# Optimization experiments

Hardware: AMD Instinct MI355X
Metric: run time of the kernel (lower is better)

The kernel has to match this reference:

```python
import jax, jax.numpy as jnp
import numpy as np

N = 4096          # residues
D = 256           # local feature dim
FACTOR = 2
H = 8             # global heads
DF = D * FACTOR   # 512
DH = DF // H      # 64 per-head dim
NUM_CHAINS = 64
NUM_BATCHES = 8


def index_mean(x, idx, mask, num_segments):
    """Masked segment mean, gathered back to per-element shape.
    x: [N, ...], idx: [N] int, mask: broadcastable to x (0/1)."""
    m = mask.astype(x.dtype)
    xm = x * m
    s = jax.ops.segment_sum(xm, idx, num_segments=num_segments)
    c = jax.ops.segment_sum(jnp.broadcast_to(m, x.shape), idx, num_segments=num_segments)
    mean = s / jnp.maximum(c, 1e-6)
    return mean[idx]


def setup_inputs() -> dict:
    key = jax.random.key(0)
    ks = jax.random.split(key, 12)
    s_in = 1.0 / np.sqrt(D)
    s_mid = 1.0 / np.sqrt(2 * DF)
    return {
        "local": jax.random.normal(ks[0], (N, D), jnp.float32),
        "chain": jax.random.randint(ks[1], (N,), 0, NUM_CHAINS),
        "batch": jax.random.randint(ks[2], (N,), 0, NUM_BATCHES),
        "mask": jax.random.bernoulli(ks[3], 0.9, (N,)),
        "W_key": jax.random.normal(ks[4], (D, DF), jnp.float32) * s_in,
        "b_key": jnp.zeros((DF,), jnp.float32),
        "W_value": jax.random.normal(ks[5], (D, DF), jnp.float32) * s_in,
        "b_value": jnp.zeros((DF,), jnp.float32),
        "W_query": jax.random.normal(ks[6], (D, DF), jnp.float32) * s_in,
        "b_query": jnp.zeros((DF,), jnp.float32),
        "W_bias": jax.random.normal(ks[7], (D, 2 * DF), jnp.float32) * s_in,
        "b_bias": jnp.zeros((2 * DF,), jnp.float32),
        "W_out": jax.random.normal(ks[8], (2 * DF, D), jnp.float32) * s_mid,
    }


def reference(local, chain, batch, mask,
              W_key, b_key, W_value, b_value, W_query, b_query,
              W_bias, b_bias, W_out):
    n = local.shape[0]
    k = jax.nn.gelu(local @ W_key + b_key).reshape(n, H, DH)
    v = (local @ W_value + b_value).reshape(n, H, DH)
    q = jax.nn.gelu(local @ W_query + b_query).reshape(n, H, DH)

    bias = index_mean(local @ W_bias + b_bias, batch, mask[:, None], NUM_BATCHES)

    # outer product key (x) value: [N, H, DH, DH]
    ov = k[:, :, :, None] * v[:, :, None, :]
    m4 = mask[:, None, None, None]
    chain_op = index_mean(ov, chain, m4, NUM_CHAINS)
    batch_op = index_mean(ov, batch, m4, NUM_BATCHES)
    operation = jnp.concatenate((chain_op, batch_op), axis=-2)  # [N, H, 2*DH, DH]

    out = jnp.einsum('bhvk,bhk->bhv', operation, q).reshape(n, -1) + bias
    return out @ W_out
```

## Files before the change

### kernel.cpp

```cpp
#include <hip/hip_runtime.h>
#include <math.h>

#define NN 4096
#define DD 256
#define DFF 512
#define HH 8
#define DHH 64
#define CAP_C 256
#define CAP_B 1024

#define OFF_KB     0
#define OFF_VB     1048576
#define OFF_QB     2097152
#define OFF_ATTNB  3145728
#define OFF_LOCALB 5242880
#define OFF_STC    5767168
#define OFF_STBP   7864320
#define OFF_BSUM   8912896
#define OFF_CNT    8921088
#define OFF_WQKVT  8921344
#define OFF_WOUTT  9117952
#define OFF_LISTS  9249024
#define OFF_LPART  9298176

typedef __attribute__((ext_vector_type(8))) short bf16x8;
typedef __attribute__((ext_vector_type(4))) float floatx4;

__device__ __forceinline__ float gelu_f(float x) {
    const float c = 0.7978845608028654f;
    float t = tanhf(c * (x + 0.044715f * x * x * x));
    return 0.5f * x * (1.0f + t);
}

__device__ __forceinline__ unsigned short f2b(float f) {
    union { float f; unsigned int u; } v; v.f = f;
    unsigned int r = (v.u + 0x7FFFu + ((v.u >> 16) & 1u)) >> 16;
    return (unsigned short)r;
}

__global__ __launch_bounds__(256) void prep_kernel(
    const float* __restrict__ local,
    const float* __restrict__ Wk, const float* __restrict__ Wv,
    const float* __restrict__ Wq, const float* __restrict__ Wout,
    const int* __restrict__ batch, const int* __restrict__ mask,
    unsigned short* __restrict__ Wqkvt, unsigned short* __restrict__ Woutt,
    unsigned short* __restrict__ localb,
    float* __restrict__ Lpart, float* __restrict__ zero_base)
{
    const int bid = blockIdx.x, tid = threadIdx.x;
    if (bid < 640) {
        const float* src; unsigned short* dst; int R, C, r0, c0;
        if (bid < 384) {
            int m = bid >> 7, ti = bid & 127;
            src = (m == 0) ? Wk : (m == 1) ? Wv : Wq;
            dst = Wqkvt + (size_t)m * 512 * 256;
            R = 256; C = 512;
            r0 = (ti >> 4) * 32; c0 = (ti & 15) * 32;
        } else {
            int ti = bid - 384;
            src = Wout; dst = Woutt;
            R = 1024; C = 256;
            r0 = (ti >> 3) * 32; c0 = (ti & 7) * 32;
        }
        __shared__ float Tl[32][33];
        int ty = tid >> 3, tx = tid & 7;
        float4 v = *(const float4*)(src + (size_t)(r0 + ty) * C + c0 + tx * 4);
        Tl[tx * 4 + 0][ty] = v.x;
        Tl[tx * 4 + 1][ty] = v.y;
        Tl[tx * 4 + 2][ty] = v.z;
        Tl[tx * 4 + 3][ty] = v.w;
        __syncthreads();
        ushort4 o;
        o.x = f2b(Tl[ty][tx * 4 + 0]);
        o.y = f2b(Tl[ty][tx * 4 + 1]);
        o.z = f2b(Tl[ty][tx * 4 + 2]);
        o.w = f2b(Tl[ty][tx * 4 + 3]);
        *(ushort4*)(dst + (size_t)(c0 + ty) * R + r0 + tx * 4) = o;
    } else if (bid < 704) {
        int p = bid - 640;
        float accl[8] = {};
        int n0 = p * 64;
        for (int r = 0; r < 64; ++r) {
            int n = n0 + r;
            float v = local[(size_t)n * DD + tid];
            int bb = batch[n];
            float vm = mask[n] ? v : 0.0f;
#pragma unroll
            for (int b = 0; b < 8; ++b)
                accl[b] += (bb == b) ? vm : 0.0f;
        }
#pragma unroll
        for (int b = 0; b < 8; ++b)
            Lpart[(size_t)p * 2048 + b * 256 + tid] = accl[b];
    } else if (bid < 1216) {
        int p = bid - 704;
        size_t base = (size_t)p * 2048 + tid * 8;
        float4 a0 = *(const float4*)(local + base);
        float4 a1 = *(const float4*)(local + base + 4);
        ushort4 p0, p1;
        p0.x = f2b(a0.x); p0.y = f2b(a0.y); p0.z = f2b(a0.z); p0.w = f2b(a0.w);
        p1.x = f2b(a1.x); p1.y = f2b(a1.y); p1.z = f2b(a1.z); p1.w = f2b(a1.w);
        *(ushort4*)(localb + base) = p0;
        *(ushort4*)(localb + base + 4) = p1;
    } else {
        float4 z4 = make_float4(0.f, 0.f, 0.f, 0.f);
        for (int i = tid; i < 2112; i += 256)
            ((float4*)zero_base)[i] = z4;
    }
}

__global__ __launch_bounds__(256) void qkv_kernel(
    const unsigned short* __restrict__ localb,
    const unsigned short* __restrict__ Wqkvt,
    const float* __restrict__ bk, const float* __restrict__ bv,
    const float* __restrict__ bq, unsigned short* __restrict__ KVQb,
    const int* __restrict__ chain, const int* __restrict__ batch,
    const int* __restrict__ mask, int* __restrict__ cnt,
    int* __restrict__ lists, const float* __restrict__ Lpart,
    const float* __restrict__ Wbias, float* __restrict__ Bsum)
{
    __shared__ __align__(16) char smem[36864];
    const int u = blockIdx.x, tid = threadIdx.x;
    int* cntc_m   = cnt;
    int* cntc_all = cnt + 64;
    int* cntb_m   = cnt + 128;
    int* cntb_all = cnt + 136;
    int* listc_m   = lists;
    int* listc_all = listc_m + 64 * CAP_C;
    int* listb_m   = listc_all + 64 * CAP_C;
    int* listb_all = listb_m + 8 * CAP_B;

    if (u < 384) {
        typedef unsigned short (*t72)[72];
        t72 Asl = (t72)smem;
        t72 Bsl = (t72)(smem + 18432);
        const int wave = tid >> 6, lane = tid & 63;
        const int kq = lane >> 4, la = lane & 15;
        const int cx = u % 12, ry = u / 12;
        const int row0 = ry * 128, cg0 = cx * 128;
        const int wrow = (wave & 1) * 64, wcol = (wave >> 1) * 64;

        floatx4 acc[4][4] = {};
        for (int kk = 0; kk < 256; kk += 64) {
#pragma unroll
            for (int t = 0; t < 4; ++t) {
                int idx = tid + t * 256;
                int rr = idx >> 3, kc = (idx & 7) * 8;
                *(float4*)&Asl[rr][kc] =
                    *(const float4*)(localb + (size_t)(row0 + rr) * DD + kk + kc);
                *(float4*)&Bsl[rr][kc] =
                    *(const float4*)(Wqkvt + (size_t)(cg0 + rr) * DD + kk + kc);
            }
            __syncthreads();
#pragma unroll
            for (int ks = 0; ks < 2; ++ks) {
                bf16x8 af[4], bf[4];
#pragma unroll
                for (int t = 0; t < 4; ++t) {
                    af[t] = *(const bf16x8*)&Asl[wrow + t * 16 + la][ks * 32 + kq * 8];
                    bf[t] = *(const bf16x8*)&Bsl[wcol + t * 16 + la][ks * 32 + kq * 8];
                }
#pragma unroll
                for (int at = 0; at < 4; ++at)
#pragma unroll
                    for (int ct = 0; ct < 4; ++ct)
                        acc[at][ct] = __builtin_amdgcn_mfma_f32_16x16x32_bf16(
                            af[at], bf[ct], acc[at][ct], 0, 0, 0);
            }
            __syncthreads();
        }
        const int sel = cg0 >> 9;
        const int do_gelu = (sel != 1);
        const float* bias = (sel == 0) ? bk : (sel == 1) ? bv : bq;
        unsigned short* C = KVQb + (size_t)sel * (NN * DFF);
#pragma unroll
        for (int ct = 0; ct < 4; ++ct) {
            int colw = (cg0 + wcol + ct * 16 + la) & 511;
            float bb = bias[colw];
#pragma unroll
            for (int at = 0; at < 4; ++at)
#pragma unroll
                for (int i = 0; i < 4; ++i) {
                    int row = row0 + wrow + at * 16 + kq * 4 + i;
                    float o = acc[at][ct][i] + bb;
                    if (do_gelu) o = gelu_f(o);
                    C[(size_t)row * DFF + colw] = f2b(o);
                }
        }
    } else if (u < 400) {
        int* sh = (int*)smem;
        int* hc_m = sh;        int* hc_all = sh + 64;
        int* hb_m = sh + 128;  int* hb_all = sh + 136;
        int* pc_m = sh + 144;  int* pc_all = sh + 208;
        int* pb_m = sh + 272;  int* pb_all = sh + 280;
        if (tid < 64) { hc_m[tid] = 0; hc_all[tid] = 0; }
        if (tid < 8)  { hb_m[tid] = 0; hb_all[tid] = 0; }
        __syncthreads();
        int n = (u - 384) * 256 + tid;
        int c = chain[n], b = batch[n], m = mask[n];
        int rc_all = atomicAdd(&hc_all[c], 1);
        int rb_all = atomicAdd(&hb_all[b], 1);
        int rc_m = -1, rb_m = -1;
        if (m) { rc_m = atomicAdd(&hc_m[c], 1); rb_m = atomicAdd(&hb_m[b], 1); }
        __syncthreads();
        if (tid < 64) {
            pc_all[tid] = atomicAdd(&cntc_all[tid], hc_all[tid]);
            pc_m[tid]   = atomicAdd(&cntc_m[tid],   hc_m[tid]);
        }
        if (tid < 8) {
            pb_all[tid] = atomicAdd(&cntb_all[tid], hb_all[tid]);
            pb_m[tid]   = atomicAdd(&cntb_m[tid],   hb_m[tid]);
        }
        __syncthreads();
        int ia = pc_all[c] + rc_all; if (ia < CAP_C) listc_all[c * CAP_C + ia] = n;
        int ib = pb_all[b] + rb_all; if (ib < CAP_B) listb_all[b * CAP_B + ib] = n;
        if (m) {
            int ja = pc_m[c] + rc_m; if (ja < CAP_C) listc_m[c * CAP_C + ja] = n;
            int jb = pb_m[b] + rb_m; if (jb < CAP_B) listb_m[b * CAP_B + jb] = n;
        }
    } else {
        int t = u - 400;
        const int seg = t >> 3, kz = t & 7;
        float (*Ltmp)[32] = (float(*)[32])smem;
        float* Lk = (float*)(smem + 8192);
        for (int idx = tid; idx < 2048; idx += 256) {
            int p = idx >> 5, k = idx & 31;
            Ltmp[p][k] = Lpart[(size_t)p * 2048 + seg * 256 + kz * 32 + k];
        }
        __syncthreads();
        if (tid < 32) {
            float s = 0.0f;
            for (int p = 0; p < 64; ++p) s += Ltmp[p][tid];
            Lk[tid] = s;
        }
        __syncthreads();
        float4 a4 = make_float4(0, 0, 0, 0);
        for (int k = 0; k < 32; ++k) {
            float l = Lk[k];
            float4 w = *(const float4*)(Wbias + (size_t)(kz * 32 + k) * 1024 + tid * 4);
            a4.x += l * w.x; a4.y += l * w.y; a4.z += l * w.z; a4.w += l * w.w;
        }
        float* o = Bsum + (size_t)seg * 1024 + tid * 4;
        atomicAdd(o + 0, a4.x); atomicAdd(o + 1, a4.y);
        atomicAdd(o + 2, a4.z); atomicAdd(o + 3, a4.w);
    }
}

__global__ __launch_bounds__(256) void mid_kernel(
    const unsigned short* __restrict__ Kb, const unsigned short* __restrict__ Vb,
    const int* __restrict__ cnt, const int* __restrict__ lists,
    float* __restrict__ STc, float* __restrict__ STbp)
{
    const int u = blockIdx.x, tid = threadIdx.x;
    const int* cntc_m = cnt;
    const int* cntb_m = cnt + 128;
    const int* listc_m = lists;
    const int* listb_m = lists + 2 * 64 * CAP_C;

    int seg, h, r0, r1, cap;
    const int* list; float* ST;
    if (u < 512) {
        seg = u >> 3; h = u & 7;
        cap = CAP_C; list = listc_m;
        r0 = 0; r1 = min(cntc_m[seg], CAP_C);
        ST = STc + ((size_t)(seg * HH + h) << 12);
    } else {
        int t = u - 512;
        int z = t >> 6; seg = (t >> 3) & 7; h = t & 7;
        cap = CAP_B; list = listb_m;
        int c = min(cntb_m[seg], CAP_B);
        int chunk = (c + 3) / 4;
        r0 = z * chunk; r1 = min(c, r0 + chunk);
        ST = STbp + (size_t)z * 262144 + ((size_t)(seg * HH + h) << 12);
    }

    __shared__ unsigned short Ktl[64][36];
    __shared__ unsigned short Vtl[64][36];
    const int wave = tid >> 6, lane = tid & 63;
    const int la = lane & 15, kq = lane >> 4;

    floatx4 acc4[4] = {};
    for (int g = r0; g < r1; g += 32) {
#pragma unroll
        for (int it = 0; it < 2; ++it) {
            int item = tid + it * 256;
            int nl = item & 31, aq = item >> 5;
            int gg = g + nl;
            ushort4 kz4 = make_ushort4(0, 0, 0, 0);
            ushort4 vz4 = make_ushort4(0, 0, 0, 0);
            if (gg < r1) {
                int nn = list[seg * cap + gg];
                kz4 = *(const ushort4*)(Kb + (size_t)nn * DFF + h * DHH + aq * 4);
                vz4 = *(const ushort4*)(Vb + (size_t)nn * DFF + h * DHH + aq * 4);
            }
            Ktl[aq * 4 + 0][nl] = kz4.x; Ktl[aq * 4 + 1][nl] = kz4.y;
            Ktl[aq * 4 + 2][nl] = kz4.z; Ktl[aq * 4 + 3][nl] = kz4.w;
            Vtl[aq * 4 + 0][nl] = vz4.x; Vtl[aq * 4 + 1][nl] = vz4.y;
            Vtl[aq * 4 + 2][nl] = vz4.z; Vtl[aq * 4 + 3][nl] = vz4.w;
        }
        __syncthreads();
        bf16x8 a = *(const bf16x8*)&Ktl[wave * 16 + la][kq * 8];
#pragma unroll
        for (int bt = 0; bt < 4; ++bt) {
            bf16x8 b = *(const bf16x8*)&Vtl[bt * 16 + la][kq * 8];
            acc4[bt] = __builtin_amdgcn_mfma_f32_16x16x32_bf16(a, b, acc4[bt], 0, 0, 0);
        }
        __syncthreads();
    }

#pragma unroll
    for (int bt = 0; bt < 4; ++bt)
#pragma unroll
        for (int rg = 0; rg < 4; ++rg) {
            int aa = wave * 16 + kq * 4 + rg;
            int bb2 = bt * 16 + la;
            ST[aa * 64 + bb2] = acc4[bt][rg];
        }
}

__global__ __launch_bounds__(256) void einsum_kernel(
    const float* __restrict__ STc, const float* __restrict__ STbp,
    const int* __restrict__ cnt, const int* __restrict__ lists,
    const unsigned short* __restrict__ Qb, const int* __restrict__ batch,
    const float* __restrict__ Bsum, const float* __restrict__ b_bias,
    unsigned short* __restrict__ attnb)
{
    const int id = blockIdx.x, tid = threadIdx.x;
    const int* cntc_m   = cnt;
    const int* cntc_all = cnt + 64;
    const int* cntb_m   = cnt + 128;
    const int* cntb_all = cnt + 136;
    const int* listc_all = lists + 64 * CAP_C;
    const int* listb_all = lists + 2 * 64 * CAP_C + 8 * CAP_B;

    int seg, h, outoff, cap, r0, r1;
    const int* list;
    float scaleS;
    bool is_chain;
    if (id < 512) {
        seg = id >> 3; h = id & 7; outoff = 0;
        list = listc_all; cap = CAP_C; is_chain = true;
        scaleS = 1.0f / fmaxf((float)min(cntc_m[seg], CAP_C), 1e-6f);
        r0 = 0; r1 = min(cntc_all[seg], CAP_C);
    } else {
        int t = id - 512;
        seg = t >> 6; h = (t >> 3) & 7;
        int z = t & 7;
        outoff = 64;
        list = listb_all; cap = CAP_B; is_chain = false;
        scaleS = 1.0f / fmaxf((float)min(cntb_m[seg], CAP_B), 1e-6f);
        int c = min(cntb_all[seg], CAP_B);
        int chunk = (c + 7) / 8;
        r0 = z * chunk; r1 = min(c, r0 + chunk);
    }

    __shared__ unsigned short Sbl[64][72];
    __shared__ unsigned short Qsl[64][72];
    __shared__ float Bf[8][64];
    __shared__ int nrow[64];
    __shared__ int nbb[64];

    const int wave = tid >> 6, lane = tid & 63;
    const int la = lane & 15, kq = lane >> 4;
    const int colbase = h * 128 + outoff;

#pragma unroll
    for (int i = 0; i < 4; ++i) {
        int e = tid + i * 256;
        float4 v;
        if (is_chain) {
            v = *(const float4*)(STc + ((size_t)(seg * HH + h) << 12) + (size_t)e * 4);
        } else {
            const float* Sg = STbp + ((size_t)(seg * HH + h) << 12) + (size_t)e * 4;
            float4 v0 = *(const float4*)(Sg);
            float4 v1 = *(const float4*)(Sg + 262144);
            float4 v2 = *(const float4*)(Sg + 524288);
            float4 v3 = *(const float4*)(Sg + 786432);
            v.x = v0.x + v1.x + v2.x + v3.x;
            v.y = v0.y + v1.y + v2.y + v3.y;
            v.z = v0.z + v1.z + v2.z + v3.z;
            v.w = v0.w + v1.w + v2.w + v3.w;
        }
        int a = e >> 4, b = (e & 15) * 4;
        ushort4 o;
        o.x = f2b(v.x * scaleS); o.y = f2b(v.y * scaleS);
        o.z = f2b(v.z * scaleS); o.w = f2b(v.w * scaleS);
        *(ushort4*)&Sbl[a][b] = o;
    }
#pragma unroll
    for (int e = tid; e < 512; e += 256) {
        int bbq = e >> 6, j = e & 63;
        float cm = (float)min(cntb_m[bbq], CAP_B);
        float inv = 1.0f / fmaxf(cm, 1e-6f);
        int col = colbase + j;
        Bf[bbq][j] = (Bsum[(size_t)bbq * 1024 + col] + cm * b_bias[col]) * inv;
    }
    __syncthreads();

    for (int g = r0; g < r1; g += 64) {
        if (tid < 64) {
            int gg = g + tid;
            int n = (gg < r1) ? list[seg * cap + gg] : -1;
            nrow[tid] = n;
            nbb[tid] = (n >= 0) ? batch[n] : 0;
        }
        __syncthreads();
        {
            int row = tid & 63, pr = tid >> 6;
            int n = nrow[row];
            if (n >= 0) {
#pragma unroll
                for (int it = 0; it < 2; ++it) {
                    int off = (pr + it * 4) * 8;
                    *(float4*)&Qsl[row][off] =
                        *(const float4*)(Qb + (size_t)n * DFF + h * DHH + off);
                }
            }
        }
        __syncthreads();

        floatx4 acc[4] = {};
#pragma unroll
        for (int ks = 0; ks < 2; ++ks) {
            bf16x8 a = *(const bf16x8*)&Qsl[wave * 16 + la][ks * 32 + kq * 8];
#pragma unroll
            for (int ct = 0; ct < 4; ++ct) {
                bf16x8 b = *(const bf16x8*)&Sbl[ct * 16 + la][ks * 32 + kq * 8];
                acc[ct] = __builtin_amdgcn_mfma_f32_16x16x32_bf16(a, b, acc[ct], 0, 0, 0);
            }
        }
#pragma unroll
        for (int ct = 0; ct < 4; ++ct)
#pragma unroll
            for (int rg = 0; rg < 4; ++rg) {
                int rowl = wave * 16 + kq * 4 + rg;
                float bias = Bf[nbb[rowl]][ct * 16 + la];
                Qsl[rowl][ct * 16 + la] = f2b(acc[ct][rg] + bias);
            }
        __syncthreads();
        {
            int row = tid & 63, pr = tid >> 6;
            int n = nrow[row];
            if (n >= 0) {
#pragma unroll
                for (int it = 0; it < 2; ++it) {
                    int off = (pr + it * 4) * 8;
                    *(float4*)(attnb + (size_t)n * 1024 + colbase + off) =
                        *(const float4*)&Qsl[row][off];
                }
            }
        }
        __syncthreads();
    }
}

__global__ __launch_bounds__(256) void mfma_gemm_final(
    const unsigned short* __restrict__ A, const unsigned short* __restrict__ Bt,
    float* __restrict__ out)
{
    const int K = 1024;
    __shared__ unsigned short Asl[32][136];
    __shared__ unsigned short Bsl[64][136];
    const int tid = threadIdx.x;
    const int wave = tid >> 6, lane = tid & 63;
    const int q = lane >> 4, r = lane & 15;
    const int row0 = blockIdx.y * 32, cg0 = blockIdx.x * 64;
    const int wrow = (wave & 1) * 16, wcol = (wave >> 1) * 32;

    floatx4 acc[2] = {};
    for (int kk = 0; kk < K; kk += 128) {
#pragma unroll
        for (int t = 0; t < 2; ++t) {
            int idx = tid + t * 256;
            int rr = idx >> 4, kc = (idx & 15) * 8;
            *(float4*)&Asl[rr][kc] = *(const float4*)(A + (size_t)(row0 + rr) * K + kk + kc);
        }
#pragma unroll
        for (int t = 0; t < 4; ++t) {
            int idx = tid + t * 256;
            int rr = idx >> 4, kc = (idx & 15) * 8;
            *(float4*)&Bsl[rr][kc] = *(const float4*)(Bt + (size_t)(cg0 + rr) * K + kk + kc);
        }
        __syncthreads();
#pragma unroll
        for (int sub = 0; sub < 4; ++sub) {
            bf16x8 a = *(const bf16x8*)&Asl[wrow + r][sub * 32 + q * 8];
#pragma unroll
            for (int c = 0; c < 2; ++c) {
                bf16x8 b = *(const bf16x8*)&Bsl[wcol + c * 16 + r][sub * 32 + q * 8];
                acc[c] = __builtin_amdgcn_mfma_f32_16x16x32_bf16(a, b, acc[c], 0, 0, 0);
            }
        }
        __syncthreads();
    }
#pragma unroll
    for (int c = 0; c < 2; ++c) {
        int col = cg0 + wcol + c * 16 + r;
#pragma unroll
        for (int i = 0; i < 4; ++i) {
            int row = row0 + wrow + q * 4 + i;
            out[(size_t)row * DD + col] = acc[c][i];
        }
    }
}

extern "C" void kernel_launch(void* const* d_in, const int* in_sizes, int n_in,
                              void* d_out, int out_size, void* d_ws, size_t ws_size,
                              hipStream_t stream)
{
    const float* local   = (const float*)d_in[0];
    const int*   chain   = (const int*)d_in[1];
    const int*   batch   = (const int*)d_in[2];
    const int*   mask    = (const int*)d_in[3];
    const float* W_key   = (const float*)d_in[4];
    const float* b_key   = (const float*)d_in[5];
    const float* W_value = (const float*)d_in[6];
    const float* b_value = (const float*)d_in[7];
    const float* W_query = (const float*)d_in[8];
    const float* b_query = (const float*)d_in[9];
    const float* W_bias  = (const float*)d_in[10];
    const float* b_bias  = (const float*)d_in[11];
    const float* W_out   = (const float*)d_in[12];
    float* out = (float*)d_out;

    float* ws = (float*)d_ws;
    unsigned short* Kb     = (unsigned short*)(ws + OFF_KB);
    unsigned short* Qb     = (unsigned short*)(ws + OFF_QB);
    unsigned short* attnb  = (unsigned short*)(ws + OFF_ATTNB);
    unsigned short* localb = (unsigned short*)(ws + OFF_LOCALB);
    float* STc    = ws + OFF_STC;
    float* STbp   = ws + OFF_STBP;
    float* Bsum   = ws + OFF_BSUM;
    int*   cnt    = (int*)(ws + OFF_CNT);
    unsigned short* Wqkvt = (unsigned short*)(ws + OFF_WQKVT);
    unsigned short* Woutt = (unsigned short*)(ws + OFF_WOUTT);
    int*   lists  = (int*)(ws + OFF_LISTS);
    float* Lpart  = ws + OFF_LPART;

    dim3 blk(256);

    prep_kernel<<<dim3(1217), blk, 0, stream>>>(
        local, W_key, W_value, W_query, W_out, batch, mask,
        Wqkvt, Woutt, localb, Lpart, ws + OFF_BSUM);

    qkv_kernel<<<dim3(464), blk, 0, stream>>>(
        localb, Wqkvt, b_key, b_value, b_query, Kb,
        chain, batch, mask, cnt, lists, Lpart, W_bias, Bsum);

    mid_kernel<<<dim3(768), blk, 0, stream>>>(
        Kb, (const unsigned short*)(ws + OFF_VB), cnt, lists, STc, STbp);

    einsum_kernel<<<dim3(1024), blk, 0, stream>>>(
        STc, STbp, cnt, lists, Qb, batch, Bsum, b_bias, attnb);

    mfma_gemm_final<<<dim3(4, 128), blk, 0, stream>>>(attnb, Woutt, out);
}
```

Baseline: 147.1 us.

## Shrink GEMM tiles and split reductions across more blocks for occupancy

The QKV GEMM tile goes from 128x128 to 64x64, taking it from 384 to 1536 blocks. The final GEMM tile shrinks to 32x32, doubling its grid. The prep bias-partial pass now has each block handle 16 rows instead of 64, making 256 partial blocks, and its reduction is two-level in the consumer. The mid kernel now schedules the larger batch-segment blocks before the chain blocks. The intent is to fill all CUs of the MI355X, at the cost of less data reuse per tile and more global loads.

```diff
diff --git a/kernel.cpp b/kernel.cpp
--- a/kernel.cpp
+++ b/kernel.cpp
@@ -76,11 +76,12 @@
         o.z = f2b(Tl[ty][tx * 4 + 2]);
         o.w = f2b(Tl[ty][tx * 4 + 3]);
         *(ushort4*)(dst + (size_t)(c0 + ty) * R + r0 + tx * 4) = o;
-    } else if (bid < 704) {
+    } else if (bid < 896) {
         int p = bid - 640;
         float accl[8] = {};
-        int n0 = p * 64;
-        for (int r = 0; r < 64; ++r) {
+        int n0 = p * 16;
+#pragma unroll
+        for (int r = 0; r < 16; ++r) {
             int n = n0 + r;
             float v = local[(size_t)n * DD + tid];
             int bb = batch[n];
@@ -92,8 +93,8 @@
 #pragma unroll
         for (int b = 0; b < 8; ++b)
             Lpart[(size_t)p * 2048 + b * 256 + tid] = accl[b];
-    } else if (bid < 1216) {
-        int p = bid - 704;
+    } else if (bid < 1408) {
+        int p = bid - 896;
         size_t base = (size_t)p * 2048 + tid * 8;
         float4 a0 = *(const float4*)(local + base);
         float4 a1 = *(const float4*)(local + base + 4);
@@ -119,7 +120,7 @@
     int* __restrict__ lists, const float* __restrict__ Lpart,
     const float* __restrict__ Wbias, float* __restrict__ Bsum)
 {
-    __shared__ __align__(16) char smem[36864];
+    __shared__ __align__(16) char smem[18944];
     const int u = blockIdx.x, tid = threadIdx.x;
     int* cntc_m   = cnt;
     int* cntc_all = cnt + 64;
@@ -130,22 +131,21 @@
     int* listb_m   = listc_all + 64 * CAP_C;
     int* listb_all = listb_m + 8 * CAP_B;
 
-    if (u < 384) {
+    if (u < 1536) {
         typedef unsigned short (*t72)[72];
         t72 Asl = (t72)smem;
-        t72 Bsl = (t72)(smem + 18432);
+        t72 Bsl = (t72)(smem + 9216);
         const int wave = tid >> 6, lane = tid & 63;
-        const int kq = lane >> 4, la = lane & 15;
-        const int cx = u % 12, ry = u / 12;
-        const int row0 = ry * 128, cg0 = cx * 128;
-        const int wrow = (wave & 1) * 64, wcol = (wave >> 1) * 64;
-
-        floatx4 acc[4][4] = {};
+        const int q = lane >> 4, r = lane & 15;
+        const int cx = u % 24, ry = u / 24;
+        const int row0 = ry * 64, cg0 = cx * 64;
+
+        floatx4 acc[4] = {};
         for (int kk = 0; kk < 256; kk += 64) {
 #pragma unroll
-            for (int t = 0; t < 4; ++t) {
-                int idx = tid + t * 256;
-                int rr = idx >> 3, kc = (idx & 7) * 8;
+            for (int i = 0; i < 2; ++i) {
+                int lin = tid * 2 + i;
+                int rr = lin >> 3, kc = (lin & 7) * 8;
                 *(float4*)&Asl[rr][kc] =
                     *(const float4*)(localb + (size_t)(row0 + rr) * DD + kk + kc);
                 *(float4*)&Bsl[rr][kc] =
@@ -153,19 +153,13 @@
             }
             __syncthreads();
 #pragma unroll
-            for (int ks = 0; ks < 2; ++ks) {
-                bf16x8 af[4], bf[4];
-#pragma unroll
-                for (int t = 0; t < 4; ++t) {
-                    af[t] = *(const bf16x8*)&Asl[wrow + t * 16 + la][ks * 32 + kq * 8];
-                    bf[t] = *(const bf16x8*)&Bsl[wcol + t * 16 + la][ks * 32 + kq * 8];
+            for (int sub = 0; sub < 2; ++sub) {
+                bf16x8 a = *(const bf16x8*)&Asl[wave * 16 + r][sub * 32 + q * 8];
+#pragma unroll
+                for (int c = 0; c < 4; ++c) {
+                    bf16x8 b = *(const bf16x8*)&Bsl[c * 16 + r][sub * 32 + q * 8];
+                    acc[c] = __builtin_amdgcn_mfma_f32_16x16x32_bf16(a, b, acc[c], 0, 0, 0);
                 }
-#pragma unroll
-                for (int at = 0; at < 4; ++at)
-#pragma unroll
-                    for (int ct = 0; ct < 4; ++ct)
-                        acc[at][ct] = __builtin_amdgcn_mfma_f32_16x16x32_bf16(
-                            af[at], bf[ct], acc[at][ct], 0, 0, 0);
             }
             __syncthreads();
         }
@@ -174,20 +168,18 @@
         const float* bias = (sel == 0) ? bk : (sel == 1) ? bv : bq;
         unsigned short* C = KVQb + (size_t)sel * (NN * DFF);
 #pragma unroll
-        for (int ct = 0; ct < 4; ++ct) {
-            int colw = (cg0 + wcol + ct * 16 + la) & 511;
+        for (int c = 0; c < 4; ++c) {
+            int colw = (cg0 + c * 16 + r) & 511;
             float bb = bias[colw];
 #pragma unroll
-            for (int at = 0; at < 4; ++at)
-#pragma unroll
-                for (int i = 0; i < 4; ++i) {
-                    int row = row0 + wrow + at * 16 + kq * 4 + i;
-                    float o = acc[at][ct][i] + bb;
-                    if (do_gelu) o = gelu_f(o);
-                    C[(size_t)row * DFF + colw] = f2b(o);
-                }
-        }
-    } else if (u < 400) {
+            for (int i = 0; i < 4; ++i) {
+                int row = row0 + wave * 16 + q * 4 + i;
+                float o = acc[c][i] + bb;
+                if (do_gelu) o = gelu_f(o);
+                C[(size_t)row * DFF + colw] = f2b(o);
+            }
+        }
+    } else if (u < 1552) {
         int* sh = (int*)smem;
         int* hc_m = sh;        int* hc_all = sh + 64;
         int* hb_m = sh + 128;  int* hb_all = sh + 136;
@@ -196,7 +188,7 @@
         if (tid < 64) { hc_m[tid] = 0; hc_all[tid] = 0; }
         if (tid < 8)  { hb_m[tid] = 0; hb_all[tid] = 0; }
         __syncthreads();
-        int n = (u - 384) * 256 + tid;
+        int n = (u - 1536) * 256 + tid;
         int c = chain[n], b = batch[n], m = mask[n];
         int rc_all = atomicAdd(&hc_all[c], 1);
         int rb_all = atomicAdd(&hb_all[b], 1);
@@ -219,18 +211,23 @@
             int jb = pb_m[b] + rb_m; if (jb < CAP_B) listb_m[b * CAP_B + jb] = n;
         }
     } else {
-        int t = u - 400;
+        int t = u - 1552;
         const int seg = t >> 3, kz = t & 7;
-        float (*Ltmp)[32] = (float(*)[32])smem;
-        float* Lk = (float*)(smem + 8192);
-        for (int idx = tid; idx < 2048; idx += 256) {
-            int p = idx >> 5, k = idx & 31;
-            Ltmp[p][k] = Lpart[(size_t)p * 2048 + seg * 256 + kz * 32 + k];
+        float (*part)[32] = (float(*)[32])smem;
+        float* Lk = (float*)(smem + 1024);
+        {
+            int k = tid & 31, pg = tid >> 5;
+            float s = 0.0f;
+#pragma unroll 8
+            for (int p = pg * 32; p < pg * 32 + 32; ++p)
+                s += Lpart[(size_t)p * 2048 + seg * 256 + kz * 32 + k];
+            part[pg][k] = s;
         }
         __syncthreads();
         if (tid < 32) {
             float s = 0.0f;
-            for (int p = 0; p < 64; ++p) s += Ltmp[p][tid];
+#pragma unroll
+            for (int pg = 0; pg < 8; ++pg) s += part[pg][tid];
             Lk[tid] = s;
         }
         __syncthreads();
@@ -259,19 +256,19 @@
 
     int seg, h, r0, r1, cap;
     const int* list; float* ST;
-    if (u < 512) {
-        seg = u >> 3; h = u & 7;
-        cap = CAP_C; list = listc_m;
-        r0 = 0; r1 = min(cntc_m[seg], CAP_C);
-        ST = STc + ((size_t)(seg * HH + h) << 12);
-    } else {
-        int t = u - 512;
-        int z = t >> 6; seg = (t >> 3) & 7; h = t & 7;
+    if (u < 256) {
+        int z = u >> 6; seg = (u >> 3) & 7; h = u & 7;
         cap = CAP_B; list = listb_m;
         int c = min(cntb_m[seg], CAP_B);
         int chunk = (c + 3) / 4;
         r0 = z * chunk; r1 = min(c, r0 + chunk);
         ST = STbp + (size_t)z * 262144 + ((size_t)(seg * HH + h) << 12);
+    } else {
+        int t = u - 256;
+        seg = t >> 3; h = t & 7;
+        cap = CAP_C; list = listc_m;
+        r0 = 0; r1 = min(cntc_m[seg], CAP_C);
+        ST = STc + ((size_t)(seg * HH + h) << 12);
     }
 
     __shared__ unsigned short Ktl[64][36];
@@ -460,47 +457,36 @@
 {
     const int K = 1024;
     __shared__ unsigned short Asl[32][136];
-    __shared__ unsigned short Bsl[64][136];
+    __shared__ unsigned short Bsl[32][136];
     const int tid = threadIdx.x;
     const int wave = tid >> 6, lane = tid & 63;
     const int q = lane >> 4, r = lane & 15;
-    const int row0 = blockIdx.y * 32, cg0 = blockIdx.x * 64;
-    const int wrow = (wave & 1) * 16, wcol = (wave >> 1) * 32;
-
-    floatx4 acc[2] = {};
+    const int row0 = blockIdx.y * 32, cg0 = blockIdx.x * 32;
+    const int wrow = (wave & 1) * 16, wcol = (wave >> 1) * 16;
+
+    floatx4 acc = {};
     for (int kk = 0; kk < K; kk += 128) {
 #pragma unroll
         for (int t = 0; t < 2; ++t) {
             int idx = tid + t * 256;
             int rr = idx >> 4, kc = (idx & 15) * 8;
             *(float4*)&Asl[rr][kc] = *(const float4*)(A + (size_t)(row0 + rr) * K + kk + kc);
-        }
-#pragma unroll
-        for (int t = 0; t < 4; ++t) {
-            int idx = tid + t * 256;
-            int rr = idx >> 4, kc = (idx & 15) * 8;
             *(float4*)&Bsl[rr][kc] = *(const float4*)(Bt + (size_t)(cg0 + rr) * K + kk + kc);
         }
         __syncthreads();
 #pragma unroll
         for (int sub = 0; sub < 4; ++sub) {
             bf16x8 a = *(const bf16x8*)&Asl[wrow + r][sub * 32 + q * 8];
-#pragma unroll
-            for (int c = 0; c < 2; ++c) {
-                bf16x8 b = *(const bf16x8*)&Bsl[wcol + c * 16 + r][sub * 32 + q * 8];
-                acc[c] = __builtin_amdgcn_mfma_f32_16x16x32_bf16(a, b, acc[c], 0, 0, 0);
-            }
-        }
-        __syncthreads();
-    }
-#pragma unroll
-    for (int c = 0; c < 2; ++c) {
-        int col = cg0 + wcol + c * 16 + r;
-#pragma unroll
-        for (int i = 0; i < 4; ++i) {
-            int row = row0 + wrow + q * 4 + i;
-            out[(size_t)row * DD + col] = acc[c][i];
-        }
+            bf16x8 b = *(const bf16x8*)&Bsl[wcol + r][sub * 32 + q * 8];
+            acc = __builtin_amdgcn_mfma_f32_16x16x32_bf16(a, b, acc, 0, 0, 0);
+        }
+        __syncthreads();
+    }
+    int col = cg0 + wcol + r;
+#pragma unroll
+    for (int i = 0; i < 4; ++i) {
+        int row = row0 + wrow + q * 4 + i;
+        out[(size_t)row * DD + col] = acc[i];
     }
 }
 
@@ -539,11 +525,11 @@
 
     dim3 blk(256);
 
-    prep_kernel<<<dim3(1217), blk, 0, stream>>>(
+    prep_kernel<<<dim3(1409), blk, 0, stream>>>(
         local, W_key, W_value, W_query, W_out, batch, mask,
         Wqkvt, Woutt, localb, Lpart, ws + OFF_BSUM);
 
-    qkv_kernel<<<dim3(464), blk, 0, stream>>>(
+    qkv_kernel<<<dim3(1616), blk, 0, stream>>>(
         localb, Wqkvt, b_key, b_value, b_query, Kb,
         chain, batch, mask, cnt, lists, Lpart, W_bias, Bsum);
 
@@ -553,5 +539,5 @@
     einsum_kernel<<<dim3(1024), blk, 0, stream>>>(
         STc, STbp, cnt, lists, Qb, batch, Bsum, b_bias, attnb);
 
-    mfma_gemm_final<<<dim3(4, 128), blk, 0, stream>>>(attnb, Woutt, out);
-}
+    mfma_gemm_final<<<dim3(8, 128), blk, 0, stream>>>(attnb, Woutt, out);
+}
```

Result: faster. 134.0 us (-8.9%).
